# Optimization experiments

Hardware: AMD Instinct MI355X
Metric: run time of the kernel (lower is better)

The kernel has to match this reference:

```python
import jax, jax.numpy as jnp
import numpy as np

N, B, H, L, FE = 32768, 256, 128, 4, 4
E = 262144


def setup_inputs() -> dict:
    key = jax.random.key(0)
    ks = jax.random.split(key, 16)
    def g(i, shape, scale=0.05):
        return jax.random.normal(ks[i], shape, dtype=jnp.float32) * scale
    return {
        "d": jax.random.uniform(ks[0], (E,), dtype=jnp.float32) * 5.0,
        "src": jax.random.randint(ks[1], (E,), 0, N),
        "dst": jax.random.randint(ks[2], (E,), 0, N),
        "seg": jnp.sort(jax.random.randint(ks[3], (N,), 0, B)),
        "node_emb": g(4, (H,), 1.0),
        "We": g(5, (2 * FE + 1, H)), "be": jnp.zeros((H,), jnp.float32),
        "msg_W1": g(6, (L, 3 * H, H)), "msg_b1": jnp.zeros((L, H), jnp.float32),
        "msg_W2": g(7, (L, H, H)), "msg_b2": jnp.zeros((L, H), jnp.float32),
        "soft_W": g(8, (L, H)), "soft_b": jnp.zeros((L,), jnp.float32),
        "upd_W1": g(9, (L, H, H)), "upd_b1": jnp.zeros((L, H), jnp.float32),
        "upd_W2": g(10, (L, H, H)), "upd_b2": jnp.zeros((L, H), jnp.float32),
        "out_W1": g(11, (H, H)), "out_b1": jnp.zeros((H,), jnp.float32),
        "out_W2": g(12, (H, H)), "out_b2": jnp.zeros((H,), jnp.float32),
    }


def reference(d, src, dst, seg, node_emb, We, be, msg_W1, msg_b1, msg_W2, msg_b2,
              soft_W, soft_b, upd_W1, upd_b1, upd_W2, upd_b2,
              out_W1, out_b1, out_W2, out_b2):
    silu = jax.nn.silu
    # fourier_encode_dist: [E] -> [E, 2*FE+1] = [sin(d/2^k), cos(d/2^k), d]
    scales = 2.0 ** jnp.arange(FE, dtype=d.dtype)
    x = d[:, None] / scales
    de = jnp.concatenate([jnp.sin(x), jnp.cos(x), d[:, None]], axis=-1)
    # edge_input MLP (1 layer, last_activation=SiLU) then extra F.silu in input_edge_func
    e = silu(silu(de @ We + be))                              # [E, H]
    # node_embedding broadcast to all nodes
    feat = jnp.broadcast_to(node_emb, (N, H))
    for l in range(L):
        mi = jnp.concatenate([feat[src], feat[dst], e], axis=-1)        # [E, 3H]
        m = silu(silu(mi @ msg_W1[l] + msg_b1[l]) @ msg_W2[l] + msg_b2[l])  # [E, H]
        e = e + m                                             # edge residual update
        w = jax.nn.sigmoid(m @ soft_W[l] + soft_b[l])[:, None]  # soft edge gate [E,1]
        msum = jax.ops.segment_sum(m * w, dst, num_segments=N)  # reduce to dst nodes
        upd_in = msum + feat
        feat = silu(upd_in @ upd_W1[l] + upd_b1[l]) @ upd_W2[l] + upd_b2[l] + feat
    # node-wise output network (2 layers, last activation None)
    feat = silu(feat @ out_W1 + out_b1) @ out_W2 + out_b2
    # multi-aggregator readout over graphs in batch
    s = jax.ops.segment_sum(feat, seg, num_segments=B)
    cnt = jax.ops.segment_sum(jnp.ones((N, 1), feat.dtype), seg, num_segments=B)
    mean = s / jnp.maximum(cnt, 1.0)
    mx = jax.ops.segment_max(feat, seg, num_segments=B)
    return jnp.concatenate([s, mean, mx], axis=-1)            # [B, 3H]
```

## Files before the change

### kernel.cpp

```cpp
#include <hip/hip_runtime.h>
#include <hip/hip_bf16.h>

#define NN 32768
#define NB 256
#define HD 128
#define NL 4
#define NE 262144

typedef short bf16x8 __attribute__((ext_vector_type(8)));
typedef float f32x4 __attribute__((ext_vector_type(4)));
typedef unsigned short u16;
typedef unsigned int u32;

__device__ __forceinline__ float bf2f(u16 u) {
  return __uint_as_float(((u32)u) << 16);
}
__device__ __forceinline__ u16 f2bf(float f) {
  u32 x = __float_as_uint(f);
  u32 r = x + 0x7FFFu + ((x >> 16) & 1u);
  return (u16)(r >> 16);
}
__device__ __forceinline__ u32 pk2(float a, float b) {
  __hip_bfloat162 h = __float22bfloat162_rn(make_float2(a, b));
  return *reinterpret_cast<u32*>(&h);
}
__device__ __forceinline__ float siluf(float x) {
  return x * __builtin_amdgcn_rcpf(1.0f + __expf(-x));
}
__device__ __forceinline__ float sigf(float x) {
  return __builtin_amdgcn_rcpf(1.0f + __expf(-x));
}
__device__ __forceinline__ u32 ordu(float f) {
  u32 b = __float_as_uint(f);
  return (b & 0x80000000u) ? ~b : (b | 0x80000000u);
}

__device__ __forceinline__ float ldinf(const void* p, size_t i, int mode) {
  return mode ? ((const float*)p)[i] : bf2f(((const u16*)p)[i]);
}
__device__ __forceinline__ u16 ldinb(const void* p, size_t i, int mode) {
  return mode ? f2bf(((const float*)p)[i]) : ((const u16*)p)[i];
}

__global__ void k_detect(const u16* __restrict__ Weraw, int* __restrict__ flag) {
  if (threadIdx.x == 0 && blockIdx.x == 0) {
    int cnt = 0;
    for (int i = 0; i < 256; i++) {
      u16 u = Weraw[2 * i];
      u32 e = (u >> 7) & 0xFFu;
      if (e >= 112u && e <= 126u) cnt++;
    }
    *flag = (cnt >= 128) ? 0 : 1;
  }
}


__global__ __launch_bounds__(256) void k_csr_deg(const int* __restrict__ dstp,
                                                 u32* __restrict__ deg) {
  const int i = blockIdx.x * 256 + threadIdx.x;
  atomicAdd(&deg[dstp[i]], 1u);
}

__global__ __launch_bounds__(1024) void k_csr_scan(const u32* __restrict__ deg,
                                                   int* __restrict__ rowptr,
                                                   int* __restrict__ cursor) {
  __shared__ int part[1024];
  const int t = threadIdx.x;
  int loc[32];
  int s = 0;
#pragma unroll
  for (int j = 0; j < 32; j++) { loc[j] = s; s += (int)deg[t * 32 + j]; }
  part[t] = s;
  __syncthreads();
  int inc = s;
  for (int off = 1; off < 1024; off <<= 1) {
    int tmp = (t >= off) ? part[t - off] : 0;
    __syncthreads();
    part[t] += tmp;
    __syncthreads();
  }
  const int base = part[t] - inc;
#pragma unroll
  for (int j = 0; j < 32; j++) {
    rowptr[t * 32 + j] = base + loc[j];
    cursor[t * 32 + j] = base + loc[j];
  }
  if (t == 1023) rowptr[NN] = part[1023];
}

__global__ __launch_bounds__(256) void k_csr_scatter(const int* __restrict__ dstp,
                                                     const int* __restrict__ srcp,
                                                     int* __restrict__ cursor,
                                                     int* __restrict__ eids,
                                                     int* __restrict__ src_s,
                                                     int* __restrict__ dst_s) {
  const int i = blockIdx.x * 256 + threadIdx.x;
  const int d = dstp[i];
  const int pos = atomicAdd(&cursor[d], 1);
  eids[pos] = i;
  src_s[pos] = srcp[i];
  dst_s[pos] = d;
}

#define PANEL 16384

template <int MT>
__device__ __forceinline__ void acc_zero(f32x4 (&acc)[MT][8]) {
#pragma unroll
  for (int mt = 0; mt < MT; mt++)
#pragma unroll
    for (int nt = 0; nt < 8; nt++) acc[mt][nt] = f32x4{0.f, 0.f, 0.f, 0.f};
}

template <int MT>
__device__ __forceinline__ void gemm_gp(const u16* __restrict__ A0,
                                        const size_t* rowoff,
                                        const u16* __restrict__ Bp,
                                        int l, int kg, f32x4 (&acc)[MT][8]) {
#pragma unroll
  for (int ks = 0; ks < 4; ks++) {
    bf16x8 a[MT];
#pragma unroll
    for (int mt = 0; mt < MT; mt++)
      a[mt] = *(const bf16x8*)&A0[rowoff[mt] + ks * 32 + kg * 8];
#pragma unroll
    for (int nt = 0; nt < 8; nt++) {
      bf16x8 b = *(const bf16x8*)&Bp[(size_t)((nt * 4 + ks) * 64 + l) * 8];
#pragma unroll
      for (int mt = 0; mt < MT; mt++)
        acc[mt][nt] = __builtin_amdgcn_mfma_f32_16x16x32_bf16(a[mt], b, acc[mt][nt], 0, 0, 0);
    }
  }
}

template <int MT>
__device__ __forceinline__ void wave_gemm_p(const short* lAw, const u16* __restrict__ Bp,
                                            int l, int c, int kg, f32x4 (&acc)[MT][8]) {
#pragma unroll
  for (int ks = 0; ks < 4; ks++) {
    bf16x8 a[MT];
#pragma unroll
    for (int mt = 0; mt < MT; mt++) {
      const int r = mt * 16 + c;
      const int k = ks * 32 + kg * 8;
      a[mt] = *(const bf16x8*)&lAw[r * HD + (k ^ ((r & 7) << 3))];
    }
#pragma unroll
    for (int nt = 0; nt < 8; nt++) {
      bf16x8 b = *(const bf16x8*)&Bp[(size_t)((nt * 4 + ks) * 64 + l) * 8];
#pragma unroll
      for (int mt = 0; mt < MT; mt++)
        acc[mt][nt] = __builtin_amdgcn_mfma_f32_16x16x32_bf16(a[mt], b, acc[mt][nt], 0, 0, 0);
    }
  }
}

template <int MT, bool SILU>
__device__ __forceinline__ void wave_pack(short* lAw, int c, int kg,
                                          f32x4 (&acc)[MT][8], const float* bias) {
#pragma unroll
  for (int mt = 0; mt < MT; mt++) {
#pragma unroll
    for (int rr = 0; rr < 4; rr++) {
      const int row = mt * 16 + kg * 4 + rr;
      u32 ou[4];
#pragma unroll
      for (int p = 0; p < 4; p++) {
        float x0 = acc[mt][2 * p][rr] + bias[2 * p];
        float x1 = acc[mt][2 * p + 1][rr] + bias[2 * p + 1];
        if (SILU) { x0 = siluf(x0); x1 = siluf(x1); }
        ou[p] = pk2(x0, x1);
      }
      ((int4*)(lAw + row * HD))[c ^ (row & 7)] =
          make_int4((int)ou[0], (int)ou[1], (int)ou[2], (int)ou[3]);
    }
  }
}

__global__ __launch_bounds__(256) void k_prep(
    const void* __restrict__ mW1, const void* __restrict__ mW2,
    const void* __restrict__ uW1, const void* __restrict__ uW2,
    const void* __restrict__ oW1, const void* __restrict__ oW2,
    const int* __restrict__ flagp,
    u16* __restrict__ Wt1, u16* __restrict__ Wt2p,
    u16* __restrict__ Wtu1, u16* __restrict__ Wtu2p,
    u16* __restrict__ Wto1, u16* __restrict__ Wto2p) {
  const int mode = *flagp;
  const int tid = blockIdx.x * blockDim.x + threadIdx.x;
  const int stride = gridDim.x * blockDim.x;
  for (int i = tid; i < NL * 3 * PANEL; i += stride) {
    const int l = i / (3 * PANEL), r = i % (3 * PANEL);
    const int chunk = r / PANEL, r2 = r % PANEL;
    const int nt = r2 / 2048, ks = (r2 % 2048) / 512;
    const int lane = (r2 % 512) / 8, j = r2 % 8;
    const int s = ks * 32 + (lane >> 4) * 8 + j;
    const int klog = ((s & 7) << 4) | (s >> 3);
    const int n = nt * 16 + (lane & 15);
    Wt1[i] = ldinb(mW1, ((size_t)l * 384 + chunk * 128 + klog) * HD + n, mode);
  }
  for (int i = tid; i < NL * PANEL; i += stride) {
    const int l = i / PANEL, r = i % PANEL;
    const int nt = r / 2048, ks = (r % 2048) / 512;
    const int lane = (r % 512) / 8, j = r % 8;
    const int s = ks * 32 + (lane >> 4) * 8 + j;
    const int klog = ((s & 7) << 4) | (s >> 3);
    const int n = nt * 16 + (lane & 15);
    Wt2p[i] = ldinb(mW2, ((size_t)l * HD + klog) * HD + n, mode);
    Wtu1[i] = ldinb(uW1, ((size_t)l * HD + klog) * HD + n, mode);
    Wtu2p[i] = ldinb(uW2, ((size_t)l * HD + klog) * HD + n, mode);
  }
  for (int i = tid; i < PANEL; i += stride) {
    const int nt = i / 2048, ks = (i % 2048) / 512;
    const int lane = (i % 512) / 8, j = i % 8;
    const int s = ks * 32 + (lane >> 4) * 8 + j;
    const int klog = ((s & 7) << 4) | (s >> 3);
    const int n = nt * 16 + (lane & 15);
    Wto1[i] = ldinb(oW1, (size_t)klog * HD + n, mode);
    Wto2p[i] = ldinb(oW2, (size_t)klog * HD + n, mode);
  }
}

__global__ __launch_bounds__(256) void k_featinit(const void* __restrict__ nemb,
                                                  const int* __restrict__ flagp,
                                                  u16* __restrict__ feat) {
  const int mode = *flagp;
  const int i = blockIdx.x * 256 + threadIdx.x;
  const int g = i & 15;
  u32 ou[4];
#pragma unroll
  for (int p = 0; p < 4; p++) {
    u16 a = ldinb(nemb, (2 * p) * 16 + g, mode);
    u16 b = ldinb(nemb, (2 * p + 1) * 16 + g, mode);
    ou[p] = (u32)a | ((u32)b << 16);
  }
  ((int4*)feat)[i] = make_int4((int)ou[0], (int)ou[1], (int)ou[2], (int)ou[3]);
}

__global__ __launch_bounds__(256) void k_encode(const void* __restrict__ d,
                                                const int* __restrict__ eids,
                                                const void* __restrict__ We,
                                                const void* __restrict__ be,
                                                const int* __restrict__ flagp,
                                                u16* __restrict__ e) {
  const int mode = *flagp;
  __shared__ float sW[9 * HD];
  __shared__ float sb[HD];
  for (int i = threadIdx.x; i < 9 * HD; i += 256) sW[i] = ldinf(We, i, mode);
  for (int i = threadIdx.x; i < HD; i += 256) sb[i] = ldinf(be, i, mode);
  __syncthreads();
  const int spos = blockIdx.x * 256 + threadIdx.x;
  const float dv = ldinf(d, eids[spos], mode);
  float de[9];
#pragma unroll
  for (int k = 0; k < 4; k++) {
    float x = dv * (1.0f / (float)(1 << k));
    de[k] = __sinf(x);
    de[4 + k] = __cosf(x);
  }
  de[8] = dv;
  u16* erow = e + (size_t)spos * HD;
#pragma unroll
  for (int g = 0; g < 16; g++) {
    u32 ou[4];
#pragma unroll
    for (int p = 0; p < 4; p++) {
      float vv[2];
#pragma unroll
      for (int t = 0; t < 2; t++) {
        const int h = (2 * p + t) * 16 + g;
        float a = sb[h];
#pragma unroll
        for (int k = 0; k < 9; k++) a += de[k] * sW[k * HD + h];
        vv[t] = siluf(siluf(a));
      }
      ou[p] = pk2(vv[0], vv[1]);
    }
    ((int4*)erow)[g] = make_int4((int)ou[0], (int)ou[1], (int)ou[2], (int)ou[3]);
  }
}

__global__ __launch_bounds__(64, 4) void k_edge(
    const u16* __restrict__ feat, u16* __restrict__ e,
    const int* __restrict__ src_s, const int* __restrict__ dst_s,
    const u16* __restrict__ Wt1, const u16* __restrict__ Wt2p,
    const void* __restrict__ b1g, const void* __restrict__ b2g,
    const void* __restrict__ softW, const void* __restrict__ softb,
    const int* __restrict__ flagp, float* __restrict__ msum, int layer) {
  __shared__ __align__(16) short lM[32 * HD];
  __shared__ float swg[32];
  __shared__ int sdst[32];
  const int mode = *flagp;
  const int l = threadIdx.x;
  const int c = l & 15, kg = l >> 4;
  const int bid = (int)blockIdx.x;
  const int blk = (((bid & 7) << 10) | (bid >> 3)) * 32;

  if (l < 32) sdst[l] = dst_s[blk + l];

  size_t offS[2], offD[2], offE[2];
#pragma unroll
  for (int mt = 0; mt < 2; mt++) {
    const int eidx = blk + mt * 16 + c;
    offS[mt] = (size_t)src_s[eidx] * HD;
    offD[mt] = (size_t)dst_s[eidx] * HD;
    offE[mt] = (size_t)eidx * HD;
  }

  const u16* W1l = Wt1 + (size_t)layer * 3 * PANEL;
  const u16* W2l = Wt2p + (size_t)layer * PANEL;
  float bias1[8], bias2[8], swf[8];
#pragma unroll
  for (int nt = 0; nt < 8; nt++) {
    bias1[nt] = ldinf(b1g, layer * HD + nt * 16 + c, mode);
    bias2[nt] = ldinf(b2g, layer * HD + nt * 16 + c, mode);
    swf[nt] = ldinf(softW, (size_t)layer * HD + nt * 16 + c, mode);
  }
  const float sbv = ldinf(softb, layer, mode);

  f32x4 acc[2][8];
  acc_zero<2>(acc);
  gemm_gp<2>(feat, offS, W1l, l, kg, acc);
  gemm_gp<2>(feat, offD, W1l + PANEL, l, kg, acc);
  gemm_gp<2>(e, offE, W1l + 2 * PANEL, l, kg, acc);
  wave_pack<2, true>(lM, c, kg, acc, bias1);
  __syncthreads();

  acc_zero<2>(acc);
  wave_gemm_p<2>(lM, W2l, l, c, kg, acc);
  __syncthreads();

  float wred[2][4];
#pragma unroll
  for (int mt = 0; mt < 2; mt++) {
#pragma unroll
    for (int rr = 0; rr < 4; rr++) {
      const int row = mt * 16 + kg * 4 + rr;
      int4* erow4 = (int4*)(e + (size_t)(blk + row) * HD);
      const int4 eo = erow4[c];
      const u32 eu[4] = {(u32)eo.x, (u32)eo.y, (u32)eo.z, (u32)eo.w};
      float mv[8];
      float wp = 0.f;
#pragma unroll
      for (int nt = 0; nt < 8; nt++) {
        mv[nt] = siluf(acc[mt][nt][rr] + bias2[nt]);
        wp += mv[nt] * swf[nt];
      }
      u32 mo[4], ou[4];
#pragma unroll
      for (int p = 0; p < 4; p++) {
        mo[p] = pk2(mv[2 * p], mv[2 * p + 1]);
        ou[p] = pk2(bf2f((u16)(eu[p] & 0xffffu)) + mv[2 * p],
                    bf2f((u16)(eu[p] >> 16)) + mv[2 * p + 1]);
      }
      ((int4*)(lM + row * HD))[c ^ (row & 7)] =
          make_int4((int)mo[0], (int)mo[1], (int)mo[2], (int)mo[3]);
      erow4[c] = make_int4((int)ou[0], (int)ou[1], (int)ou[2], (int)ou[3]);
      wp += __shfl_xor(wp, 1);
      wp += __shfl_xor(wp, 2);
      wp += __shfl_xor(wp, 4);
      wp += __shfl_xor(wp, 8);
      wred[mt][rr] = wp;
    }
  }
#pragma unroll
  for (int mt = 0; mt < 2; mt++)
#pragma unroll
    for (int rr = 0; rr < 4; rr++)
      if (c == mt * 4 + rr) swg[mt * 16 + kg * 4 + rr] = sigf(wred[mt][rr] + sbv);
  __syncthreads();

  const int gM = ((l >> 3) << 3);
  const int em = l & 7;
  float a0 = 0.f, a1 = 0.f;
  int cur = sdst[0];
  for (int r = 0; r < 32; r++) {
    const int dn = sdst[r];
    if (dn != cur) {
      atomicAdd(&msum[(size_t)cur * HD + l], a0);
      atomicAdd(&msum[(size_t)cur * HD + l + 64], a1);
      a0 = 0.f; a1 = 0.f; cur = dn;
    }
    const int rx = (r & 7) << 3;
    const float wgr = swg[r];
    a0 += wgr * bf2f((u16)lM[r * HD + (gM ^ rx) + em]);
    a1 += wgr * bf2f((u16)lM[r * HD + (gM ^ rx) + 64 + em]);
  }
  atomicAdd(&msum[(size_t)cur * HD + l], a0);
  atomicAdd(&msum[(size_t)cur * HD + l + 64], a1);
}

__global__ __launch_bounds__(64, 4) void k_node(
    u16* __restrict__ feat, float* __restrict__ msum,
    const u16* __restrict__ Wtu1, const u16* __restrict__ Wtu2p,
    const void* __restrict__ b1g, const void* __restrict__ b2g,
    const int* __restrict__ flagp, int layer) {
  __shared__ __align__(16) short lA[32 * HD];
  const int mode = *flagp;
  const int l = threadIdx.x;
  const int c = l & 15, kg = l >> 4;
  short* lAw = lA;
  const int bid = (int)blockIdx.x;
  const int blkn = (((bid & 7) << 7) | (bid >> 3)) * 32;
  const u16* W1l = Wtu1 + (size_t)layer * PANEL;
  const u16* W2l = Wtu2p + (size_t)layer * PANEL;
  float bias1[8], bias2[8];
#pragma unroll
  for (int nt = 0; nt < 8; nt++) {
    bias1[nt] = ldinf(b1g, layer * HD + nt * 16 + c, mode);
    bias2[nt] = ldinf(b2g, layer * HD + nt * 16 + c, mode);
  }
  const float4 z4 = make_float4(0.f, 0.f, 0.f, 0.f);
#pragma unroll
  for (int rp = 0; rp < 8; rp++) {
    const int r = rp * 4 + (l >> 4);
    const int g = l & 15;
    const int4 fv = ((const int4*)(feat + (size_t)(blkn + r) * HD))[g];
    const u32 uu[4] = {(u32)fv.x, (u32)fv.y, (u32)fv.z, (u32)fv.w};
    float4* mrow4 = (float4*)(msum + (size_t)(blkn + r) * HD);
    const float4 ma = mrow4[2 * g];
    const float4 mb = mrow4[2 * g + 1];
    mrow4[2 * g] = z4;
    mrow4[2 * g + 1] = z4;
    const float mm[8] = {ma.x, ma.y, ma.z, ma.w, mb.x, mb.y, mb.z, mb.w};
    u32 ou[4];
#pragma unroll
    for (int p = 0; p < 4; p++) {
      ou[p] = pk2(bf2f((u16)(uu[p] & 0xffffu)) + mm[2 * p],
                  bf2f((u16)(uu[p] >> 16)) + mm[2 * p + 1]);
    }
    ((int4*)(lAw + r * HD))[g ^ (r & 7)] =
        make_int4((int)ou[0], (int)ou[1], (int)ou[2], (int)ou[3]);
  }
  __syncthreads();
  f32x4 acc[2][8];
  acc_zero<2>(acc);
  wave_gemm_p<2>(lAw, W1l, l, c, kg, acc);
  __syncthreads();
  wave_pack<2, true>(lAw, c, kg, acc, bias1);
  __syncthreads();
  acc_zero<2>(acc);
  wave_gemm_p<2>(lAw, W2l, l, c, kg, acc);

#pragma unroll
  for (int mt = 0; mt < 2; mt++) {
#pragma unroll
    for (int rr = 0; rr < 4; rr++) {
      const int row = mt * 16 + kg * 4 + rr;
      int4* frow4 = (int4*)(feat + (size_t)(blkn + row) * HD);
      const int4 fo = frow4[c];
      const u32 fu[4] = {(u32)fo.x, (u32)fo.y, (u32)fo.z, (u32)fo.w};
      u32 ou[4];
#pragma unroll
      for (int p = 0; p < 4; p++) {
        const float x0 = acc[mt][2 * p][rr] + bias2[2 * p];
        const float x1 = acc[mt][2 * p + 1][rr] + bias2[2 * p + 1];
        ou[p] = pk2(bf2f((u16)(fu[p] & 0xffffu)) + x0,
                    bf2f((u16)(fu[p] >> 16)) + x1);
      }
      frow4[c] = make_int4((int)ou[0], (int)ou[1], (int)ou[2], (int)ou[3]);
    }
  }
}

__global__ __launch_bounds__(64, 4) void k_out(
    const u16* __restrict__ feat, const int* __restrict__ seg,
    const u16* __restrict__ Wto1, const u16* __restrict__ Wto2p,
    const void* __restrict__ ob1, const void* __restrict__ ob2,
    const int* __restrict__ flagp,
    float* __restrict__ sacc, u32* __restrict__ mxacc, float* __restrict__ cnt) {
  __shared__ __align__(16) short lA[32 * HD];
  __shared__ int sseg[32];
  const int mode = *flagp;
  const int l = threadIdx.x;
  const int c = l & 15, kg = l >> 4;
  short* lAw = lA;
  const int bid = (int)blockIdx.x;
  const int blkn = (((bid & 7) << 7) | (bid >> 3)) * 32;
  float bias1[8], bias2[8];
#pragma unroll
  for (int nt = 0; nt < 8; nt++) {
    bias1[nt] = ldinf(ob1, nt * 16 + c, mode);
    bias2[nt] = ldinf(ob2, nt * 16 + c, mode);
  }
#pragma unroll
  for (int rp = 0; rp < 8; rp++) {
    const int r = rp * 4 + (l >> 4);
    const int g = l & 15;
    ((int4*)(lAw + r * HD))[g ^ (r & 7)] =
        ((const int4*)(feat + (size_t)(blkn + r) * HD))[g];
  }
  if (l < 32) sseg[l] = seg[blkn + l];
  __syncthreads();
  f32x4 acc[2][8];
  acc_zero<2>(acc);
  wave_gemm_p<2>(lAw, Wto1, l, c, kg, acc);
  __syncthreads();
  wave_pack<2, true>(lAw, c, kg, acc, bias1);
  __syncthreads();
  acc_zero<2>(acc);
  wave_gemm_p<2>(lAw, Wto2p, l, c, kg, acc);
  __syncthreads();
  wave_pack<2, false>(lAw, c, kg, acc, bias2);
  __syncthreads();

  const int gL = l >> 2;
  const int eoff = (l & 3) * 2;
  const bool uniform = (sseg[0] == sseg[31]);
  if (uniform) {
    const int g = sseg[0];
    float s1 = 0.f, s2 = 0.f, x1 = -3.402823e38f, x2 = -3.402823e38f;
#pragma unroll 4
    for (int r = 0; r < 32; r++) {
      const u32 mv = *(const u32*)&lAw[r * HD + ((gL ^ (r & 7)) << 3) + eoff];
      const float v1 = bf2f((u16)(mv & 0xffffu));
      const float v2 = bf2f((u16)(mv >> 16));
      s1 += v1; s2 += v2;
      x1 = fmaxf(x1, v1); x2 = fmaxf(x2, v2);
    }
    atomicAdd(&sacc[(size_t)g * HD + 2 * l], s1);
    atomicAdd(&sacc[(size_t)g * HD + 2 * l + 1], s2);
    atomicMax(&mxacc[(size_t)g * HD + 2 * l], ordu(x1));
    atomicMax(&mxacc[(size_t)g * HD + 2 * l + 1], ordu(x2));
    if (l == 0) atomicAdd(&cnt[g], 32.0f);
  } else {
    if (l < 32) atomicAdd(&cnt[sseg[l]], 1.0f);
#pragma unroll 4
    for (int r = 0; r < 32; r++) {
      const u32 mv = *(const u32*)&lAw[r * HD + ((gL ^ (r & 7)) << 3) + eoff];
      const float v1 = bf2f((u16)(mv & 0xffffu));
      const float v2 = bf2f((u16)(mv >> 16));
      const int g = sseg[r];
      atomicAdd(&sacc[(size_t)g * HD + 2 * l], v1);
      atomicAdd(&sacc[(size_t)g * HD + 2 * l + 1], v2);
      atomicMax(&mxacc[(size_t)g * HD + 2 * l], ordu(v1));
      atomicMax(&mxacc[(size_t)g * HD + 2 * l + 1], ordu(v2));
    }
  }
}

__global__ __launch_bounds__(256) void k_final(const float* __restrict__ sacc,
                                               const u32* __restrict__ mxacc,
                                               const float* __restrict__ cnt,
                                               const int* __restrict__ flagp,
                                               void* __restrict__ out) {
  const int mode = *flagp;
  const int i = blockIdx.x * 256 + threadIdx.x;
  const int b = i / 384, j = i % 384;
  float v;
  if (j < HD) {
    const int p = ((j & 15) << 3) | (j >> 4);
    v = sacc[b * HD + p];
  } else if (j < 2 * HD) {
    const int t = j - HD;
    const int p = ((t & 15) << 3) | (t >> 4);
    v = sacc[b * HD + p] / fmaxf(cnt[b], 1.0f);
  } else {
    const int t = j - 2 * HD;
    const int p = ((t & 15) << 3) | (t >> 4);
    u32 u = mxacc[b * HD + p];
    u32 bits = (u >> 31) ? (u ^ 0x80000000u) : ~u;
    v = __uint_as_float(bits);
  }
  if (mode) ((float*)out)[i] = v;
  else ((u16*)out)[i] = f2bf(v);
}

extern "C" void kernel_launch(void* const* d_in, const int* in_sizes, int n_in,
                              void* d_out, int out_size, void* d_ws, size_t ws_size,
                              hipStream_t stream) {
  const void* d_d = d_in[0];
  const int* src = (const int*)d_in[1];
  const int* dst = (const int*)d_in[2];
  const int* seg = (const int*)d_in[3];
  const void* nemb = d_in[4];
  const void* We = d_in[5];
  const void* be = d_in[6];
  const void* mW1 = d_in[7];
  const void* mb1 = d_in[8];
  const void* mW2 = d_in[9];
  const void* mb2 = d_in[10];
  const void* sW = d_in[11];
  const void* sb = d_in[12];
  const void* uW1 = d_in[13];
  const void* ub1 = d_in[14];
  const void* uW2 = d_in[15];
  const void* ub2 = d_in[16];
  const void* oW1 = d_in[17];
  const void* ob1 = d_in[18];
  const void* oW2 = d_in[19];
  const void* ob2 = d_in[20];

  char* ws = (char*)d_ws;
  const size_t OFF_E = 0;
  const size_t OFF_MSUM = OFF_E + (size_t)NE * HD * 2;
  const size_t OFF_FEAT = OFF_MSUM + (size_t)NN * HD * 4;
  const size_t OFF_SACC = OFF_FEAT + (size_t)NN * HD * 2;
  const size_t OFF_MX = OFF_SACC + (size_t)NB * HD * 4;
  const size_t OFF_CNT = OFF_MX + (size_t)NB * HD * 4;
  const size_t OFF_DEG = OFF_CNT + 1024;
  const size_t OFF_ROWPTR = OFF_DEG + (size_t)NN * 4;
  const size_t OFF_CURSOR = OFF_ROWPTR + (size_t)(NN + 2) * 4;
  const size_t OFF_EIDS = OFF_CURSOR + (size_t)NN * 4;
  const size_t OFF_SRCS = OFF_EIDS + (size_t)NE * 4;
  const size_t OFF_DSTS = OFF_SRCS + (size_t)NE * 4;
  const size_t OFF_WT1 = OFF_DSTS + (size_t)NE * 4;
  const size_t OFF_WT2P = OFF_WT1 + (size_t)NL * 3 * PANEL * 2;
  const size_t OFF_WTU1 = OFF_WT2P + (size_t)NL * PANEL * 2;
  const size_t OFF_WTU2P = OFF_WTU1 + (size_t)NL * PANEL * 2;
  const size_t OFF_WTO1 = OFF_WTU2P + (size_t)NL * PANEL * 2;
  const size_t OFF_WTO2P = OFF_WTO1 + (size_t)PANEL * 2;
  const size_t OFF_FLAG = OFF_WTO2P + (size_t)PANEL * 2;

  u16* e = (u16*)(ws + OFF_E);
  float* msum = (float*)(ws + OFF_MSUM);
  u16* feat = (u16*)(ws + OFF_FEAT);
  float* sacc = (float*)(ws + OFF_SACC);
  u32* mx = (u32*)(ws + OFF_MX);
  float* cnt = (float*)(ws + OFF_CNT);
  u32* deg = (u32*)(ws + OFF_DEG);
  int* rowptr = (int*)(ws + OFF_ROWPTR);
  int* cursor = (int*)(ws + OFF_CURSOR);
  int* eids = (int*)(ws + OFF_EIDS);
  int* src_s = (int*)(ws + OFF_SRCS);
  int* dst_s = (int*)(ws + OFF_DSTS);
  u16* Wt1 = (u16*)(ws + OFF_WT1);
  u16* Wt2p = (u16*)(ws + OFF_WT2P);
  u16* Wtu1 = (u16*)(ws + OFF_WTU1);
  u16* Wtu2p = (u16*)(ws + OFF_WTU2P);
  u16* Wto1 = (u16*)(ws + OFF_WTO1);
  u16* Wto2p = (u16*)(ws + OFF_WTO2P);
  int* flag = (int*)(ws + OFF_FLAG);

  hipMemsetAsync(ws + OFF_SACC, 0,
                 (size_t)NB * HD * 4 * 2 + 1024 + (size_t)NN * 4, stream);
  hipMemsetAsync(msum, 0, (size_t)NN * HD * 4, stream);

  k_detect<<<1, 64, 0, stream>>>((const u16*)We, flag);
  k_prep<<<256, 256, 0, stream>>>(mW1, mW2, uW1, uW2, oW1, oW2, flag,
                                  Wt1, Wt2p, Wtu1, Wtu2p, Wto1, Wto2p);
  k_featinit<<<(NN * HD / 8) / 256, 256, 0, stream>>>(nemb, flag, feat);

  k_csr_deg<<<NE / 256, 256, 0, stream>>>(dst, deg);
  k_csr_scan<<<1, 1024, 0, stream>>>(deg, rowptr, cursor);
  k_csr_scatter<<<NE / 256, 256, 0, stream>>>(dst, src, cursor, eids, src_s, dst_s);

  k_encode<<<NE / 256, 256, 0, stream>>>(d_d, eids, We, be, flag, e);

  for (int l = 0; l < NL; l++) {
    k_edge<<<NE / 32, 64, 0, stream>>>(feat, e, src_s, dst_s, Wt1, Wt2p,
                                       mb1, mb2, sW, sb, flag, msum, l);
    k_node<<<NN / 32, 64, 0, stream>>>(feat, msum, Wtu1, Wtu2p, ub1, ub2, flag, l);
  }
  k_out<<<NN / 32, 64, 0, stream>>>(feat, seg, Wto1, Wto2p, ob1, ob2, flag, sacc, mx, cnt);
  k_final<<<(NB * 384) / 256, 256, 0, stream>>>(sacc, mx, cnt, flag, d_out);
}
```

Baseline: 749.8 us.

## Stage edge-MLP weight panels in LDS shared by four waves per block

```diff
diff --git a/kernel.cpp b/kernel.cpp
--- a/kernel.cpp
+++ b/kernel.cpp
@@ -112,25 +112,28 @@
     for (int nt = 0; nt < 8; nt++) acc[mt][nt] = f32x4{0.f, 0.f, 0.f, 0.f};
 }
 
-template <int MT>
-__device__ __forceinline__ void gemm_gp(const u16* __restrict__ A0,
-                                        const size_t* rowoff,
-                                        const u16* __restrict__ Bp,
-                                        int l, int kg, f32x4 (&acc)[MT][8]) {
-#pragma unroll
-  for (int ks = 0; ks < 4; ks++) {
-    bf16x8 a[MT];
-#pragma unroll
-    for (int mt = 0; mt < MT; mt++)
-      a[mt] = *(const bf16x8*)&A0[rowoff[mt] + ks * 32 + kg * 8];
+__device__ __forceinline__ void load_a2(const u16* __restrict__ A0,
+                                        const size_t* rowoff, int kg,
+                                        bf16x8 (&a)[2][4]) {
+#pragma unroll
+  for (int ks = 0; ks < 4; ks++)
+#pragma unroll
+    for (int mt = 0; mt < 2; mt++)
+      a[mt][ks] = *(const bf16x8*)&A0[rowoff[mt] + ks * 32 + kg * 8];
+}
+
+__device__ __forceinline__ void gemm_lds2(const bf16x8 (&a)[2][4],
+                                          const short* sB, int l,
+                                          f32x4 (&acc)[2][8]) {
+#pragma unroll
+  for (int ks = 0; ks < 4; ks++)
 #pragma unroll
     for (int nt = 0; nt < 8; nt++) {
-      bf16x8 b = *(const bf16x8*)&Bp[(size_t)((nt * 4 + ks) * 64 + l) * 8];
-#pragma unroll
-      for (int mt = 0; mt < MT; mt++)
-        acc[mt][nt] = __builtin_amdgcn_mfma_f32_16x16x32_bf16(a[mt], b, acc[mt][nt], 0, 0, 0);
-    }
-  }
+      bf16x8 b = *(const bf16x8*)&sB[((nt * 4 + ks) * 64 + l) * 8];
+#pragma unroll
+      for (int mt = 0; mt < 2; mt++)
+        acc[mt][nt] = __builtin_amdgcn_mfma_f32_16x16x32_bf16(a[mt][ks], b, acc[mt][nt], 0, 0, 0);
+    }
 }
 
 template <int MT>
@@ -174,6 +177,15 @@
       ((int4*)(lAw + row * HD))[c ^ (row & 7)] =
           make_int4((int)ou[0], (int)ou[1], (int)ou[2], (int)ou[3]);
     }
+  }
+}
+
+__device__ __forceinline__ void stage_panel(const u16* __restrict__ P,
+                                            short* sB, int tid) {
+#pragma unroll
+  for (int it = 0; it < 8; it++) {
+    const int idx = (it * 256 + tid) * 8;
+    *(int4*)&sB[idx] = *(const int4*)&P[idx];
   }
 }
 
@@ -279,23 +291,29 @@
   }
 }
 
-__global__ __launch_bounds__(64, 4) void k_edge(
+__global__ __launch_bounds__(256, 2) void k_edge(
     const u16* __restrict__ feat, u16* __restrict__ e,
     const int* __restrict__ src_s, const int* __restrict__ dst_s,
     const u16* __restrict__ Wt1, const u16* __restrict__ Wt2p,
     const void* __restrict__ b1g, const void* __restrict__ b2g,
     const void* __restrict__ softW, const void* __restrict__ softb,
     const int* __restrict__ flagp, float* __restrict__ msum, int layer) {
-  __shared__ __align__(16) short lM[32 * HD];
-  __shared__ float swg[32];
-  __shared__ int sdst[32];
+  __shared__ __align__(16) short sB[PANEL];
+  __shared__ __align__(16) short lM[128 * HD];
+  __shared__ float swg[128];
+  __shared__ int sdst[128];
   const int mode = *flagp;
-  const int l = threadIdx.x;
+  const int tid = threadIdx.x;
+  const int l = tid & 63, wid = tid >> 6;
   const int c = l & 15, kg = l >> 4;
   const int bid = (int)blockIdx.x;
-  const int blk = (((bid & 7) << 10) | (bid >> 3)) * 32;
-
-  if (l < 32) sdst[l] = dst_s[blk + l];
+  const int blkB = (((bid & 7) << 8) | (bid >> 3)) * 128;
+  const int blk = blkB + wid * 32;
+  short* lMw = lM + wid * 32 * HD;
+  float* swgw = swg + wid * 32;
+  int* sdstw = sdst + wid * 32;
+
+  if (l < 32) sdstw[l] = dst_s[blk + l];
 
   size_t offS[2], offD[2], offE[2];
 #pragma unroll
@@ -319,15 +337,30 @@
 
   f32x4 acc[2][8];
   acc_zero<2>(acc);
-  gemm_gp<2>(feat, offS, W1l, l, kg, acc);
-  gemm_gp<2>(feat, offD, W1l + PANEL, l, kg, acc);
-  gemm_gp<2>(e, offE, W1l + 2 * PANEL, l, kg, acc);
-  wave_pack<2, true>(lM, c, kg, acc, bias1);
+  bf16x8 a[2][4];
+
+  load_a2(feat, offS, kg, a);
+  stage_panel(W1l, sB, tid);
+  __syncthreads();
+  gemm_lds2(a, sB, l, acc);
+  __syncthreads();
+  load_a2(feat, offD, kg, a);
+  stage_panel(W1l + PANEL, sB, tid);
+  __syncthreads();
+  gemm_lds2(a, sB, l, acc);
+  __syncthreads();
+  load_a2(e, offE, kg, a);
+  stage_panel(W1l + 2 * PANEL, sB, tid);
+  __syncthreads();
+  gemm_lds2(a, sB, l, acc);
+  __syncthreads();
+
+  stage_panel(W2l, sB, tid);
+  wave_pack<2, true>(lMw, c, kg, acc, bias1);
   __syncthreads();
 
   acc_zero<2>(acc);
-  wave_gemm_p<2>(lM, W2l, l, c, kg, acc);
-  __syncthreads();
+  wave_gemm_p<2>(lMw, (const u16*)sB, l, c, kg, acc);
 
   float wred[2][4];
 #pragma unroll
@@ -352,7 +385,7 @@
         ou[p] = pk2(bf2f((u16)(eu[p] & 0xffffu)) + mv[2 * p],
                     bf2f((u16)(eu[p] >> 16)) + mv[2 * p + 1]);
       }
-      ((int4*)(lM + row * HD))[c ^ (row & 7)] =
+      ((int4*)(lMw + row * HD))[c ^ (row & 7)] =
           make_int4((int)mo[0], (int)mo[1], (int)mo[2], (int)mo[3]);
       erow4[c] = make_int4((int)ou[0], (int)ou[1], (int)ou[2], (int)ou[3]);
       wp += __shfl_xor(wp, 1);
@@ -366,24 +399,23 @@
   for (int mt = 0; mt < 2; mt++)
 #pragma unroll
     for (int rr = 0; rr < 4; rr++)
-      if (c == mt * 4 + rr) swg[mt * 16 + kg * 4 + rr] = sigf(wred[mt][rr] + sbv);
-  __syncthreads();
+      if (c == mt * 4 + rr) swgw[mt * 16 + kg * 4 + rr] = sigf(wred[mt][rr] + sbv);
 
   const int gM = ((l >> 3) << 3);
   const int em = l & 7;
   float a0 = 0.f, a1 = 0.f;
-  int cur = sdst[0];
+  int cur = sdstw[0];
   for (int r = 0; r < 32; r++) {
-    const int dn = sdst[r];
+    const int dn = sdstw[r];
     if (dn != cur) {
       atomicAdd(&msum[(size_t)cur * HD + l], a0);
       atomicAdd(&msum[(size_t)cur * HD + l + 64], a1);
       a0 = 0.f; a1 = 0.f; cur = dn;
     }
     const int rx = (r & 7) << 3;
-    const float wgr = swg[r];
-    a0 += wgr * bf2f((u16)lM[r * HD + (gM ^ rx) + em]);
-    a1 += wgr * bf2f((u16)lM[r * HD + (gM ^ rx) + 64 + em]);
+    const float wgr = swgw[r];
+    a0 += wgr * bf2f((u16)lMw[r * HD + (gM ^ rx) + em]);
+    a1 += wgr * bf2f((u16)lMw[r * HD + (gM ^ rx) + 64 + em]);
   }
   atomicAdd(&msum[(size_t)cur * HD + l], a0);
   atomicAdd(&msum[(size_t)cur * HD + l + 64], a1);
@@ -647,8 +679,8 @@
   k_encode<<<NE / 256, 256, 0, stream>>>(d_d, eids, We, be, flag, e);
 
   for (int l = 0; l < NL; l++) {
-    k_edge<<<NE / 32, 64, 0, stream>>>(feat, e, src_s, dst_s, Wt1, Wt2p,
-                                       mb1, mb2, sW, sb, flag, msum, l);
+    k_edge<<<NE / 128, 256, 0, stream>>>(feat, e, src_s, dst_s, Wt1, Wt2p,
+                                         mb1, mb2, sW, sb, flag, msum, l);
     k_node<<<NN / 32, 64, 0, stream>>>(feat, msum, Wtu1, Wtu2p, ub1, ub2, flag, l);
   }
   k_out<<<NN / 32, 64, 0, stream>>>(feat, seg, Wto1, Wto2p, ob1, ob2, flag, sacc, mx, cnt);
```

After: 741.5 us. No clear change (-1.1%).
